# Kernel optimization log

Hardware: AMD Instinct MI355X
Metric: run time of the kernel (lower is better)

The kernel has to match this reference:

```python
import jax, jax.numpy as jnp
import numpy as np

# Graph / model dims (see init_kwargs)
N = 50000          # nodes
E = 800000         # edges (before self loops)
IN, HID, OUT = 128, 64, 47
HEADS = (4, 4, 1)
SLOPE = 0.2        # PyG GATConv default negative_slope
# dropout p=0.6 in the torch module is a no-op in eval mode -> omitted


def _glorot(key, shape):
    fan_in = shape[0] if len(shape) == 2 else int(np.prod(shape))
    return jax.random.normal(key, shape, jnp.float32) / np.sqrt(fan_in)


def setup_inputs() -> dict:
    key = jax.random.key(0)
    ks = jax.random.split(key, 16)
    x = jax.random.normal(ks[0], (N, IN), jnp.float32)
    edge_index = jax.random.randint(ks[1], (2, E), 0, N)
    # layer dims: (in_dim, out_dim_per_head, heads)
    dims = [(IN, HID, HEADS[0]), (HID * HEADS[0], HID, HEADS[1]), (HID * HEADS[1], OUT, HEADS[2])]
    inp = {"x": x, "edge_index": edge_index}
    for i, (d_in, c, h) in enumerate(dims, start=1):
        inp[f"W{i}"] = _glorot(ks[3 * i], (d_in, h * c))
        inp[f"a{i}s"] = _glorot(ks[3 * i + 1], (h, c))
        inp[f"a{i}d"] = _glorot(ks[3 * i + 2], (h, c))
        inp[f"b{i}"] = jnp.zeros((h * c,), jnp.float32)
    return inp


def gat_layer(x, src, dst, W, a_s, a_d, b, h, c):
    # x: [N, d_in] -> per-head features [N, h, c]
    feat = (x @ W).reshape(N, h, c)
    # per-node attention logits [N, h]
    al_src = jnp.einsum('nhc,hc->nh', feat, a_s)
    al_dst = jnp.einsum('nhc,hc->nh', feat, a_d)
    # per-edge score, LeakyReLU (PyG: alpha = a_src[src] + a_dst[dst])
    e = jax.nn.leaky_relu(al_src[src] + al_dst[dst], SLOPE)  # [Etot, h]
    # segment softmax over incoming edges of each dst node
    emax = jax.ops.segment_max(e, dst, num_segments=N)       # [N, h]
    w = jnp.exp(e - emax[dst])
    denom = jax.ops.segment_sum(w, dst, num_segments=N)      # [N, h]
    alpha = w / denom[dst]                                   # [Etot, h]
    # weighted scatter-add aggregation
    out = jax.ops.segment_sum(alpha[:, :, None] * feat[src], dst, num_segments=N)
    return out.reshape(N, h * c) + b                         # concat heads + bias


def reference(x, edge_index, W1, a1s, a1d, b1, W2, a2s, a2d, b2, W3, a3s, a3d, b3):
    loop = jnp.arange(N, dtype=edge_index.dtype)
    src = jnp.concatenate([edge_index[0], loop])  # add_self_loops=True
    dst = jnp.concatenate([edge_index[1], loop])
    h = gat_layer(x, src, dst, W1, a1s, a1d, b1, HEADS[0], HID)
    h = jax.nn.elu(h)
    h = gat_layer(h, src, dst, W2, a2s, a2d, b2, HEADS[1], HID)
    h = jax.nn.elu(h)
    h = gat_layer(h, src, dst, W3, a3s, a3d, b3, HEADS[2], OUT)  # no elu on last layer
    return h
```

## Files before the change

kernel.cpp:

```cpp
#include <hip/hip_runtime.h>
#include <hip/hip_bf16.h>

#define NNODES 50000
#define NEDGES 800000
#define ETOT   (NNODES + NEDGES)
#define MTILES 3136
#define MPAD   (MTILES * 16)
#define NBLK   196

typedef __attribute__((ext_vector_type(8))) short short8;
typedef __attribute__((ext_vector_type(4))) float floatx4;
typedef __attribute__((ext_vector_type(2))) unsigned int uint2v;

__device__ __forceinline__ float bf2f(__hip_bfloat16 x) { return __bfloat162float(x); }
__device__ __forceinline__ __hip_bfloat16 f2bf(float f) { return __float2bfloat16(f); }
__device__ __forceinline__ float sane(float v, float c) {
  v = (v == v) ? v : 0.f;
  return fminf(fmaxf(v, -c), c);
}

__global__ void zero_int_kernel(int* __restrict__ p, int n) {
  int i = blockIdx.x * blockDim.x + threadIdx.x;
  if (i < n) p[i] = 0;
}
__global__ void fill_out_kernel(float* __restrict__ o, int n, float v) {
  int i = blockIdx.x * blockDim.x + threadIdx.x;
  if (i < n) o[i] = v;
}
__global__ void split_input_kernel(const float* __restrict__ in,
                                   __hip_bfloat16* __restrict__ hi,
                                   __hip_bfloat16* __restrict__ lo, int n) {
  int i = blockIdx.x * blockDim.x + threadIdx.x;
  if (i >= n) return;
  float v = sane(in[i], 1e4f);
  __hip_bfloat16 h = f2bf(v);
  hi[i] = h;
  lo[i] = f2bf(v - bf2f(h));
}
__global__ void zero_tail_kernel(__hip_bfloat16* __restrict__ hi,
                                 __hip_bfloat16* __restrict__ lo) {
  const int base = NNODES * 128;
  const int cnt = MPAD * 256 - base;
  int i = blockIdx.x * blockDim.x + threadIdx.x;
  if (i >= cnt) return;
  hi[base + i] = f2bf(0.f);
  lo[base + i] = f2bf(0.f);
}
__global__ void pad47_kernel(const float* __restrict__ a, const float* __restrict__ b,
                             float* __restrict__ ap, float* __restrict__ bp) {
  int i = threadIdx.x;
  ap[i] = (i < 47) ? sane(a[i], 1e4f) : 0.f;
  bp[i] = (i < 47) ? sane(b[i], 1e4f) : 0.f;
}

__global__ void degree_kernel(const int* __restrict__ ei, int* __restrict__ deg) {
  int p = blockIdx.x * blockDim.x + threadIdx.x;
  if (p >= ETOT) return;
  int dst = (p < NEDGES) ? ei[NEDGES + p] : (p - NEDGES);
  dst = min(max(dst, 0), NNODES - 1);
  atomicAdd(&deg[dst], 1);
}

__global__ __launch_bounds__(256) void block_sum_kernel(const int* __restrict__ deg,
                                                        int* __restrict__ bsum) {
  __shared__ int sh[256];
  int b = blockIdx.x, t = threadIdx.x;
  int i = b * 256 + t;
  sh[t] = (i < NNODES) ? deg[i] : 0;
  __syncthreads();
  for (int off = 128; off > 0; off >>= 1) {
    if (t < off) sh[t] += sh[t + off];
    __syncthreads();
  }
  if (t == 0) bsum[b] = sh[0];
}

__global__ __launch_bounds__(256) void scan_bsum_kernel(const int* __restrict__ bsum,
                                                        int* __restrict__ boff,
                                                        int* __restrict__ row_ptr) {
  __shared__ int sh[256];
  int t = threadIdx.x;
  int v = (t < NBLK) ? bsum[t] : 0;
  sh[t] = v;
  __syncthreads();
  for (int off = 1; off < 256; off <<= 1) {
    int u = (t >= off) ? sh[t - off] : 0;
    __syncthreads();
    sh[t] += u;
    __syncthreads();
  }
  if (t < NBLK) boff[t] = sh[t] - v;
  if (t == 255) row_ptr[NNODES] = sh[255];
}

__global__ __launch_bounds__(256) void emit_rowptr_kernel(const int* __restrict__ deg,
                                                          const int* __restrict__ boff,
                                                          int* __restrict__ row_ptr,
                                                          int* __restrict__ cursor) {
  __shared__ int sh[256];
  int b = blockIdx.x, t = threadIdx.x;
  int i = b * 256 + t;
  int d = (i < NNODES) ? deg[i] : 0;
  sh[t] = d;
  __syncthreads();
  for (int off = 1; off < 256; off <<= 1) {
    int u = (t >= off) ? sh[t - off] : 0;
    __syncthreads();
    sh[t] += u;
    __syncthreads();
  }
  if (i < NNODES) {
    int v = boff[b] + sh[t] - d;
    row_ptr[i] = v;
    cursor[i] = v;
  }
}

__global__ void scatter_kernel(const int* __restrict__ ei, int* __restrict__ cursor,
                               int* __restrict__ csr_src) {
  int p = blockIdx.x * blockDim.x + threadIdx.x;
  if (p >= ETOT) return;
  int src, dst;
  if (p < NEDGES) { src = ei[p]; dst = ei[NEDGES + p]; }
  else            { src = p - NEDGES; dst = src; }
  src = min(max(src, 0), NNODES - 1);
  dst = min(max(dst, 0), NNODES - 1);
  int pos = atomicAdd(&cursor[dst], 1);
  pos = min(max(pos, 0), ETOT - 1);
  csr_src[pos] = src;
}

__global__ void pack_w_kernel(const float* __restrict__ W,
                              __hip_bfloat16* __restrict__ Bh,
                              __hip_bfloat16* __restrict__ Bl,
                              int K, int Nreal, int Npad) {
  int idx = blockIdx.x * blockDim.x + threadIdx.x;
  if (idx >= Npad * K) return;
  int e = idx;
  int j = e & 7;    e >>= 3;
  int m = e & 15;   e >>= 4;
  int quad = e & 3; e >>= 2;
  int kch = K >> 5;
  int kk32 = e % kch;
  int nt = e / kch;
  int n = nt * 16 + m;
  int k = kk32 * 32 + quad * 8 + j;
  float v = (n < Nreal) ? sane(W[k * Nreal + n], 1e4f) : 0.f;
  __hip_bfloat16 h = f2bf(v);
  Bh[idx] = h;
  Bl[idx] = f2bf(v - bf2f(h));
}

template<int KDIM, int NOUT, int HEADS, int WAVES_N>
__global__ __launch_bounds__(256) void gemm_attn_kernel(
    const __hip_bfloat16* __restrict__ Ah, const __hip_bfloat16* __restrict__ Al,
    const __hip_bfloat16* __restrict__ Bh, const __hip_bfloat16* __restrict__ Bl,
    const float* __restrict__ asv, const float* __restrict__ adv,
    __hip_bfloat16* __restrict__ Ch, float* __restrict__ als, float* __restrict__ ald) {
  constexpr int KCH = KDIM / 32;
  constexpr int CT = (NOUT / 16) / WAVES_N;
  constexpr int RT = 4;
  constexpr int RGROUPS = 4 / WAVES_N;
  __shared__ __hip_bfloat16 sAh[64 * 32];
  __shared__ __hip_bfloat16 sAl[64 * 32];
  int wave = threadIdx.x >> 6, lane = threadIdx.x & 63;
  int wrow = wave / WAVES_N, wcol = wave % WAVES_N;
  int rt0 = (blockIdx.x * RGROUPS + wrow) * RT;
  int ct0 = wcol * CT;
  int m = lane & 15, quad = lane >> 4;

  const short8* Bph = reinterpret_cast<const short8*>(Bh);
  const short8* Bpl = reinterpret_cast<const short8*>(Bl);

  floatx4 acc[RT][CT];
#pragma unroll
  for (int rt = 0; rt < RT; ++rt)
#pragma unroll
    for (int ct = 0; ct < CT; ++ct) acc[rt][ct] = (floatx4){0.f, 0.f, 0.f, 0.f};

  int tid = threadIdx.x;
  size_t gstage = (size_t)(rt0 * 16 + (tid >> 2)) * KDIM + (tid & 3) * 8;

#pragma unroll 2
  for (int kk = 0; kk < KCH; ++kk) {
    short8 a_h[RT], a_l[RT];
    if constexpr (WAVES_N == 4) {
      short8 vh = *reinterpret_cast<const short8*>(Ah + gstage + kk * 32);
      short8 vl = *reinterpret_cast<const short8*>(Al + gstage + kk * 32);
      __syncthreads();
      *reinterpret_cast<short8*>(&sAh[tid * 8]) = vh;
      *reinterpret_cast<short8*>(&sAl[tid * 8]) = vl;
      __syncthreads();
#pragma unroll
      for (int rt = 0; rt < RT; ++rt) {
        int so = (rt * 16 + m) * 32 + quad * 8;
        a_h[rt] = *reinterpret_cast<const short8*>(&sAh[so]);
        a_l[rt] = *reinterpret_cast<const short8*>(&sAl[so]);
      }
    } else {
#pragma unroll
      for (int rt = 0; rt < RT; ++rt) {
        size_t aoff = (size_t)((rt0 + rt) * 16 + m) * KDIM + kk * 32 + quad * 8;
        a_h[rt] = *reinterpret_cast<const short8*>(Ah + aoff);
        a_l[rt] = *reinterpret_cast<const short8*>(Al + aoff);
      }
    }
#pragma unroll
    for (int ct = 0; ct < CT; ++ct) {
      size_t o = ((size_t)(ct0 + ct) * KCH + kk) * 64 + lane;
      short8 b_h = Bph[o];
      short8 b_l = Bpl[o];
#pragma unroll
      for (int rt = 0; rt < RT; ++rt) {
        acc[rt][ct] = __builtin_amdgcn_mfma_f32_16x16x32_bf16(a_h[rt], b_h, acc[rt][ct], 0, 0, 0);
        acc[rt][ct] = __builtin_amdgcn_mfma_f32_16x16x32_bf16(a_h[rt], b_l, acc[rt][ct], 0, 0, 0);
        acc[rt][ct] = __builtin_amdgcn_mfma_f32_16x16x32_bf16(a_l[rt], b_h, acc[rt][ct], 0, 0, 0);
      }
    }
  }

  constexpr int CPH = NOUT / HEADS;
  int head = (ct0 * 16) / CPH;
  float asl[CT], adl[CT];
#pragma unroll
  for (int ct = 0; ct < CT; ++ct) {
    asl[ct] = asv[(ct0 + ct) * 16 + m];
    adl[ct] = adv[(ct0 + ct) * 16 + m];
  }
  float ps[RT * 4], pd[RT * 4];
#pragma unroll
  for (int i = 0; i < RT * 4; ++i) { ps[i] = 0.f; pd[i] = 0.f; }
#pragma unroll
  for (int rt = 0; rt < RT; ++rt)
#pragma unroll
    for (int ct = 0; ct < CT; ++ct)
#pragma unroll
      for (int r = 0; r < 4; ++r) {
        ps[rt * 4 + r] += acc[rt][ct][r] * asl[ct];
        pd[rt * 4 + r] += acc[rt][ct][r] * adl[ct];
      }
#pragma unroll
  for (int off = 1; off < 16; off <<= 1) {
#pragma unroll
    for (int i = 0; i < RT * 4; ++i) {
      ps[i] += __shfl_xor(ps[i], off);
      pd[i] += __shfl_xor(pd[i], off);
    }
  }
  if (m == 0) {
#pragma unroll
    for (int rt = 0; rt < RT; ++rt)
#pragma unroll
      for (int r = 0; r < 4; ++r) {
        int row = (rt0 + rt) * 16 + quad * 4 + r;
        if (row < NNODES) {
          als[(size_t)row * HEADS + head] = sane(ps[rt * 4 + r], 80.f);
          ald[(size_t)row * HEADS + head] = sane(pd[rt * 4 + r], 80.f);
        }
      }
  }

#pragma unroll
  for (int rt = 0; rt < RT; ++rt)
#pragma unroll
    for (int ct = 0; ct < CT; ++ct)
#pragma unroll
      for (int r = 0; r < 4; ++r) {
        int row = (rt0 + rt) * 16 + quad * 4 + r;
        if (row < NNODES) {
          float v = sane(acc[rt][ct][r], 3e4f);
          Ch[(size_t)row * NOUT + (ct0 + ct) * 16 + m] = f2bf(v);
        }
      }
}

template<int H>
__global__ __launch_bounds__(256) void alpha_kernel(const int* __restrict__ row_ptr,
                                                    const int* __restrict__ csr_src,
                                                    const float* __restrict__ als,
                                                    const float* __restrict__ ald,
                                                    float* __restrict__ alpha) {
  int wid = threadIdx.x >> 6, lane = threadIdx.x & 63;
  int dst = blockIdx.x * 4 + wid;
  if (dst >= NNODES) return;
  int start = row_ptr[dst], end = row_ptr[dst + 1];
  int cnt = end - start;
  if (cnt <= 0) return;
  float adv[H];
#pragma unroll
  for (int h = 0; h < H; ++h) adv[h] = ald[(size_t)dst * H + h];

  if (cnt <= 64) {
    int i = start + lane;
    bool valid = lane < cnt;
    int s = valid ? min(max(csr_src[i], 0), NNODES - 1) : 0;
    float w[H];
#pragma unroll
    for (int h = 0; h < H; ++h) {
      float e = als[(size_t)s * H + h] + adv[h];
      e = e > 0.f ? e : 0.2f * e;
      e = fminf(fmaxf(e, -80.f), 80.f);
      w[h] = valid ? __expf(e) : 0.f;
    }
#pragma unroll
    for (int h = 0; h < H; ++h) {
      float v = w[h];
#pragma unroll
      for (int off = 1; off < 64; off <<= 1) v += __shfl_xor(v, off);
      float inv = 1.f / fmaxf(v, 1e-30f);
      if (valid) alpha[(size_t)i * H + h] = w[h] * inv;
    }
  } else {
    float dl[H];
#pragma unroll
    for (int h = 0; h < H; ++h) dl[h] = 0.f;
    for (int base = start; base < end; base += 64) {
      int i = base + lane;
      bool valid = i < end;
      int s = valid ? min(max(csr_src[i], 0), NNODES - 1) : 0;
#pragma unroll
      for (int h = 0; h < H; ++h) {
        float e = als[(size_t)s * H + h] + adv[h];
        e = e > 0.f ? e : 0.2f * e;
        e = fminf(fmaxf(e, -80.f), 80.f);
        float w = valid ? __expf(e) : 0.f;
        dl[h] += w;
        if (valid) alpha[(size_t)i * H + h] = w;
      }
    }
    float inv[H];
#pragma unroll
    for (int h = 0; h < H; ++h) {
      float v = dl[h];
#pragma unroll
      for (int off = 1; off < 64; off <<= 1) v += __shfl_xor(v, off);
      inv[h] = 1.f / fmaxf(v, 1e-30f);
    }
    for (int base = start; base < end; base += 64) {
      int i = base + lane;
      if (i < end)
#pragma unroll
        for (int h = 0; h < H; ++h) alpha[(size_t)i * H + h] *= inv[h];
    }
  }
}

__global__ __launch_bounds__(256) void agg_mid_kernel(const int* __restrict__ row_ptr,
                                                      const int* __restrict__ csr_src,
                                                      const __hip_bfloat16* __restrict__ Fh,
                                                      const float* __restrict__ alpha,
                                                      const float* __restrict__ bias,
                                                      __hip_bfloat16* __restrict__ Oh,
                                                      __hip_bfloat16* __restrict__ Ol) {
  __shared__ float part[4][256];
  int dst = blockIdx.x;
  int wid = threadIdx.x >> 6, lane = threadIdx.x & 63;
  int start = row_ptr[dst], end = row_ptr[dst + 1];
  int cnt = end - start;
  int head = lane >> 4;
  float a0 = 0.f, a1 = 0.f, a2 = 0.f, a3 = 0.f;
  int p = wid;
  for (; p + 4 < cnt; p += 8) {
    int e0 = start + p, e1 = start + p + 4;
    int s0 = csr_src[e0], s1 = csr_src[e1];
    float w0 = alpha[(size_t)e0 * 4 + head];
    float w1 = alpha[(size_t)e1 * 4 + head];
    uint2v f0 = *reinterpret_cast<const uint2v*>(Fh + (size_t)s0 * 256 + lane * 4);
    uint2v f1 = *reinterpret_cast<const uint2v*>(Fh + (size_t)s1 * 256 + lane * 4);
    a0 += w0 * __uint_as_float(f0.x << 16);
    a1 += w0 * __uint_as_float(f0.x & 0xffff0000u);
    a2 += w0 * __uint_as_float(f0.y << 16);
    a3 += w0 * __uint_as_float(f0.y & 0xffff0000u);
    a0 += w1 * __uint_as_float(f1.x << 16);
    a1 += w1 * __uint_as_float(f1.x & 0xffff0000u);
    a2 += w1 * __uint_as_float(f1.y << 16);
    a3 += w1 * __uint_as_float(f1.y & 0xffff0000u);
  }
  for (; p < cnt; p += 4) {
    int e0 = start + p;
    int s0 = csr_src[e0];
    float w0 = alpha[(size_t)e0 * 4 + head];
    uint2v f0 = *reinterpret_cast<const uint2v*>(Fh + (size_t)s0 * 256 + lane * 4);
    a0 += w0 * __uint_as_float(f0.x << 16);
    a1 += w0 * __uint_as_float(f0.x & 0xffff0000u);
    a2 += w0 * __uint_as_float(f0.y << 16);
    a3 += w0 * __uint_as_float(f0.y & 0xffff0000u);
  }
  *reinterpret_cast<floatx4*>(&part[wid][lane * 4]) = (floatx4){a0, a1, a2, a3};
  __syncthreads();
  int t = threadIdx.x;
  float o = part[0][t] + part[1][t] + part[2][t] + part[3][t] + bias[t];
  o = o > 0.f ? o : __expf(o) - 1.f;
  __hip_bfloat16 h = f2bf(o);
  Oh[(size_t)dst * 256 + t] = h;
  Ol[(size_t)dst * 256 + t] = f2bf(o - bf2f(h));
}

__global__ void agg_final_kernel(const int* __restrict__ row_ptr,
                                 const int* __restrict__ csr_src,
                                 const __hip_bfloat16* __restrict__ Fh,
                                 const float* __restrict__ alpha,
                                 const float* __restrict__ bias,
                                 float* __restrict__ out) {
  int wid = threadIdx.x >> 6, lane = threadIdx.x & 63;
  int dst = blockIdx.x * 4 + wid;
  if (dst >= NNODES) return;
  int start = row_ptr[dst], end = row_ptr[dst + 1];
  float acc = 0.f;
  int e = start;
  for (; e + 1 < end; e += 2) {
    int s0 = csr_src[e], s1 = csr_src[e + 1];
    float w0 = alpha[e], w1 = alpha[e + 1];
    float f0 = bf2f(Fh[(size_t)s0 * 64 + lane]);
    float f1 = bf2f(Fh[(size_t)s1 * 64 + lane]);
    acc += w0 * f0 + w1 * f1;
  }
  for (; e < end; ++e) {
    int s0 = csr_src[e];
    acc += alpha[e] * bf2f(Fh[(size_t)s0 * 64 + lane]);
  }
  if (lane < 47) out[(size_t)dst * 47 + lane] = acc + bias[lane];
}

extern "C" void kernel_launch(void* const* d_in, const int* in_sizes, int n_in,
                              void* d_out, int out_size, void* d_ws, size_t ws_size,
                              hipStream_t stream) {
  const float* x   = (const float*)d_in[0];
  const int* ei    = (const int*)d_in[1];
  const float* W1  = (const float*)d_in[2];
  const float* a1s = (const float*)d_in[3];
  const float* a1d = (const float*)d_in[4];
  const float* b1  = (const float*)d_in[5];
  const float* W2  = (const float*)d_in[6];
  const float* a2s = (const float*)d_in[7];
  const float* a2d = (const float*)d_in[8];
  const float* b2  = (const float*)d_in[9];
  const float* W3  = (const float*)d_in[10];
  const float* a3s = (const float*)d_in[11];
  const float* a3d = (const float*)d_in[12];
  const float* b3  = (const float*)d_in[13];
  float* out = (float*)d_out;
  (void)n_in; (void)in_sizes;

  char* base = (char*)d_ws;
  size_t off = 0;
  auto alloc = [&](size_t bytes) -> char* {
    off = (off + 255) & ~(size_t)255;
    char* p = base + off;
    off += bytes;
    return p;
  };
  int* deg     = (int*)alloc((size_t)NNODES * 4);
  int* cursor  = (int*)alloc((size_t)NNODES * 4);
  int* row_ptr = (int*)alloc((size_t)(NNODES + 1) * 4);
  int* csr_src = (int*)alloc((size_t)ETOT * 4);
  int* bsum    = (int*)alloc(256 * 4);
  int* boff    = (int*)alloc(256 * 4);
  float* als   = (float*)alloc((size_t)NNODES * 4 * 4);
  float* ald   = (float*)alloc((size_t)NNODES * 4 * 4);
  float* alpha = (float*)alloc((size_t)ETOT * 4 * 4);
  __hip_bfloat16* Ah = (__hip_bfloat16*)alloc((size_t)MPAD * 256 * 2);
  __hip_bfloat16* Al = (__hip_bfloat16*)alloc((size_t)MPAD * 256 * 2);
  __hip_bfloat16* Fh = (__hip_bfloat16*)alloc((size_t)NNODES * 256 * 2);
  __hip_bfloat16* wth = (__hip_bfloat16*)alloc((size_t)256 * 256 * 2);
  __hip_bfloat16* wtl = (__hip_bfloat16*)alloc((size_t)256 * 256 * 2);
  float* asv3 = (float*)alloc(64 * 4);
  float* adv3 = (float*)alloc(64 * 4);

  if (ws_size < off) {
    fill_out_kernel<<<(out_size + 255) / 256, 256, 0, stream>>>(out, out_size, 12345.f);
    return;
  }

  zero_int_kernel<<<(NNODES + 255) / 256, 256, 0, stream>>>(deg, NNODES);
  degree_kernel<<<(ETOT + 255) / 256, 256, 0, stream>>>(ei, deg);
  block_sum_kernel<<<NBLK, 256, 0, stream>>>(deg, bsum);
  scan_bsum_kernel<<<1, 256, 0, stream>>>(bsum, boff, row_ptr);
  emit_rowptr_kernel<<<NBLK, 256, 0, stream>>>(deg, boff, row_ptr, cursor);
  scatter_kernel<<<(ETOT + 255) / 256, 256, 0, stream>>>(ei, cursor, csr_src);

  split_input_kernel<<<(NNODES * 128 + 255) / 256, 256, 0, stream>>>(x, Ah, Al, NNODES * 128);
  {
    const int tail = MPAD * 256 - NNODES * 128;
    zero_tail_kernel<<<(tail + 255) / 256, 256, 0, stream>>>(Ah, Al);
  }
  pad47_kernel<<<1, 64, 0, stream>>>(a3s, a3d, asv3, adv3);

  const int grid12 = (NNODES + 63) / 64;
  const int grid3 = (NNODES + 255) / 256;

  pack_w_kernel<<<(256 * 128 + 255) / 256, 256, 0, stream>>>(W1, wth, wtl, 128, 256, 256);
  gemm_attn_kernel<128, 256, 4, 4><<<grid12, 256, 0, stream>>>(Ah, Al, wth, wtl, a1s, a1d,
                                                               Fh, als, ald);
  alpha_kernel<4><<<(NNODES + 3) / 4, 256, 0, stream>>>(row_ptr, csr_src, als, ald, alpha);
  agg_mid_kernel<<<NNODES, 256, 0, stream>>>(row_ptr, csr_src, Fh, alpha, b1, Ah, Al);

  pack_w_kernel<<<(256 * 256 + 255) / 256, 256, 0, stream>>>(W2, wth, wtl, 256, 256, 256);
  gemm_attn_kernel<256, 256, 4, 4><<<grid12, 256, 0, stream>>>(Ah, Al, wth, wtl, a2s, a2d,
                                                               Fh, als, ald);
  alpha_kernel<4><<<(NNODES + 3) / 4, 256, 0, stream>>>(row_ptr, csr_src, als, ald, alpha);
  agg_mid_kernel<<<NNODES, 256, 0, stream>>>(row_ptr, csr_src, Fh, alpha, b2, Ah, Al);

  pack_w_kernel<<<(64 * 256 + 255) / 256, 256, 0, stream>>>(W3, wth, wtl, 256, 47, 64);
  gemm_attn_kernel<256, 64, 1, 1><<<grid3, 256, 0, stream>>>(Ah, Al, wth, wtl, asv3, adv3,
                                                             Fh, als, ald);
  alpha_kernel<1><<<(NNODES + 3) / 4, 256, 0, stream>>>(row_ptr, csr_src, als, ald, alpha);
  agg_final_kernel<<<(NNODES + 3) / 4, 256, 0, stream>>>(row_ptr, csr_src, Fh, alpha, b3, out);
}
```

Before: 574.8 us.

## Use one wave per node in aggregation, stage two K-chunks per sync, fuse tail zeroing

The mid-layer aggregation now gives each destination node one wave instead of a 256-thread block. This removes the shared-memory partial reduction and the block barrier, and the output is written as vectorized 4-element bf16 hi/lo stores. The GEMM stages two 32-wide K chunks per pair of barriers using a double-sized LDS buffer, which halves synchronization count. The edge loops are unrolled by 4 for more memory-level parallelism, and the tail-zero kernel is folded into the split-input kernel. The per-wave design trades intra-node parallelism for less sync overhead, and high-degree nodes now run serially in a single wave.

New measurement: 515.8 us. 10.3% less time.

```diff
diff --git a/kernel.cpp b/kernel.cpp
--- a/kernel.cpp
+++ b/kernel.cpp
@@ -11,6 +11,7 @@
 typedef __attribute__((ext_vector_type(8))) short short8;
 typedef __attribute__((ext_vector_type(4))) float floatx4;
 typedef __attribute__((ext_vector_type(2))) unsigned int uint2v;
+typedef __attribute__((ext_vector_type(4))) short short4v;
 
 __device__ __forceinline__ float bf2f(__hip_bfloat16 x) { return __bfloat162float(x); }
 __device__ __forceinline__ __hip_bfloat16 f2bf(float f) { return __float2bfloat16(f); }
@@ -18,6 +19,11 @@
   v = (v == v) ? v : 0.f;
   return fminf(fmaxf(v, -c), c);
 }
+__device__ __forceinline__ unsigned short bfbits(float f) {
+  union { __hip_bfloat16 b; unsigned short u; } cv;
+  cv.b = f2bf(f);
+  return cv.u;
+}
 
 __global__ void zero_int_kernel(int* __restrict__ p, int n) {
   int i = blockIdx.x * blockDim.x + threadIdx.x;
@@ -29,22 +35,13 @@
 }
 __global__ void split_input_kernel(const float* __restrict__ in,
                                    __hip_bfloat16* __restrict__ hi,
-                                   __hip_bfloat16* __restrict__ lo, int n) {
+                                   __hip_bfloat16* __restrict__ lo) {
   int i = blockIdx.x * blockDim.x + threadIdx.x;
-  if (i >= n) return;
-  float v = sane(in[i], 1e4f);
+  if (i >= MPAD * 256) return;
+  float v = (i < NNODES * 128) ? sane(in[i], 1e4f) : 0.f;
   __hip_bfloat16 h = f2bf(v);
   hi[i] = h;
   lo[i] = f2bf(v - bf2f(h));
-}
-__global__ void zero_tail_kernel(__hip_bfloat16* __restrict__ hi,
-                                 __hip_bfloat16* __restrict__ lo) {
-  const int base = NNODES * 128;
-  const int cnt = MPAD * 256 - base;
-  int i = blockIdx.x * blockDim.x + threadIdx.x;
-  if (i >= cnt) return;
-  hi[base + i] = f2bf(0.f);
-  lo[base + i] = f2bf(0.f);
 }
 __global__ void pad47_kernel(const float* __restrict__ a, const float* __restrict__ b,
                              float* __restrict__ ap, float* __restrict__ bp) {
@@ -161,8 +158,8 @@
   constexpr int CT = (NOUT / 16) / WAVES_N;
   constexpr int RT = 4;
   constexpr int RGROUPS = 4 / WAVES_N;
-  __shared__ __hip_bfloat16 sAh[64 * 32];
-  __shared__ __hip_bfloat16 sAl[64 * 32];
+  __shared__ __hip_bfloat16 sAh[2 * 64 * 32];
+  __shared__ __hip_bfloat16 sAl[2 * 64 * 32];
   int wave = threadIdx.x >> 6, lane = threadIdx.x & 63;
   int wrow = wave / WAVES_N, wcol = wave % WAVES_N;
   int rt0 = (blockIdx.x * RGROUPS + wrow) * RT;
@@ -182,39 +179,63 @@
   size_t gstage = (size_t)(rt0 * 16 + (tid >> 2)) * KDIM + (tid & 3) * 8;
 
 #pragma unroll 2
-  for (int kk = 0; kk < KCH; ++kk) {
+  for (int ks = 0; ks < KCH / 2; ++ks) {
     short8 a_h[RT], a_l[RT];
     if constexpr (WAVES_N == 4) {
-      short8 vh = *reinterpret_cast<const short8*>(Ah + gstage + kk * 32);
-      short8 vl = *reinterpret_cast<const short8*>(Al + gstage + kk * 32);
+      short8 vh0 = *reinterpret_cast<const short8*>(Ah + gstage + ks * 64);
+      short8 vh1 = *reinterpret_cast<const short8*>(Ah + gstage + ks * 64 + 32);
+      short8 vl0 = *reinterpret_cast<const short8*>(Al + gstage + ks * 64);
+      short8 vl1 = *reinterpret_cast<const short8*>(Al + gstage + ks * 64 + 32);
       __syncthreads();
-      *reinterpret_cast<short8*>(&sAh[tid * 8]) = vh;
-      *reinterpret_cast<short8*>(&sAl[tid * 8]) = vl;
+      *reinterpret_cast<short8*>(&sAh[tid * 8]) = vh0;
+      *reinterpret_cast<short8*>(&sAh[2048 + tid * 8]) = vh1;
+      *reinterpret_cast<short8*>(&sAl[tid * 8]) = vl0;
+      *reinterpret_cast<short8*>(&sAl[2048 + tid * 8]) = vl1;
       __syncthreads();
 #pragma unroll
-      for (int rt = 0; rt < RT; ++rt) {
-        int so = (rt * 16 + m) * 32 + quad * 8;
-        a_h[rt] = *reinterpret_cast<const short8*>(&sAh[so]);
-        a_l[rt] = *reinterpret_cast<const short8*>(&sAl[so]);
+      for (int kk0 = 0; kk0 < 2; ++kk0) {
+#pragma unroll
+        for (int rt = 0; rt < RT; ++rt) {
+          int so = kk0 * 2048 + (rt * 16 + m) * 32 + quad * 8;
+          a_h[rt] = *reinterpret_cast<const short8*>(&sAh[so]);
+          a_l[rt] = *reinterpret_cast<const short8*>(&sAl[so]);
+        }
+        int kk = ks * 2 + kk0;
+#pragma unroll
+        for (int ct = 0; ct < CT; ++ct) {
+          size_t o = ((size_t)(ct0 + ct) * KCH + kk) * 64 + lane;
+          short8 b_h = Bph[o];
+          short8 b_l = Bpl[o];
+#pragma unroll
+          for (int rt = 0; rt < RT; ++rt) {
+            acc[rt][ct] = __builtin_amdgcn_mfma_f32_16x16x32_bf16(a_h[rt], b_h, acc[rt][ct], 0, 0, 0);
+            acc[rt][ct] = __builtin_amdgcn_mfma_f32_16x16x32_bf16(a_h[rt], b_l, acc[rt][ct], 0, 0, 0);
+            acc[rt][ct] = __builtin_amdgcn_mfma_f32_16x16x32_bf16(a_l[rt], b_h, acc[rt][ct], 0, 0, 0);
+          }
+        }
       }
     } else {
 #pragma unroll
-      for (int rt = 0; rt < RT; ++rt) {
-        size_t aoff = (size_t)((rt0 + rt) * 16 + m) * KDIM + kk * 32 + quad * 8;
-        a_h[rt] = *reinterpret_cast<const short8*>(Ah + aoff);
-        a_l[rt] = *reinterpret_cast<const short8*>(Al + aoff);
-      }
-    }
-#pragma unroll
-    for (int ct = 0; ct < CT; ++ct) {
-      size_t o = ((size_t)(ct0 + ct) * KCH + kk) * 64 + lane;
-      short8 b_h = Bph[o];
-      short8 b_l = Bpl[o];
-#pragma unroll
-      for (int rt = 0; rt < RT; ++rt) {
-        acc[rt][ct] = __builtin_amdgcn_mfma_f32_16x16x32_bf16(a_h[rt], b_h, acc[rt][ct], 0, 0, 0);
-        acc[rt][ct] = __builtin_amdgcn_mfma_f32_16x16x32_bf16(a_h[rt], b_l, acc[rt][ct], 0, 0, 0);
-        acc[rt][ct] = __builtin_amdgcn_mfma_f32_16x16x32_bf16(a_l[rt], b_h, acc[rt][ct], 0, 0, 0);
+      for (int kk0 = 0; kk0 < 2; ++kk0) {
+        int kk = ks * 2 + kk0;
+#pragma unroll
+        for (int rt = 0; rt < RT; ++rt) {
+          size_t aoff = (size_t)((rt0 + rt) * 16 + m) * KDIM + kk * 32 + quad * 8;
+          a_h[rt] = *reinterpret_cast<const short8*>(Ah + aoff);
+          a_l[rt] = *reinterpret_cast<const short8*>(Al + aoff);
+        }
+#pragma unroll
+        for (int ct = 0; ct < CT; ++ct) {
+          size_t o = ((size_t)(ct0 + ct) * KCH + kk) * 64 + lane;
+          short8 b_h = Bph[o];
+          short8 b_l = Bpl[o];
+#pragma unroll
+          for (int rt = 0; rt < RT; ++rt) {
+            acc[rt][ct] = __builtin_amdgcn_mfma_f32_16x16x32_bf16(a_h[rt], b_h, acc[rt][ct], 0, 0, 0);
+            acc[rt][ct] = __builtin_amdgcn_mfma_f32_16x16x32_bf16(a_h[rt], b_l, acc[rt][ct], 0, 0, 0);
+            acc[rt][ct] = __builtin_amdgcn_mfma_f32_16x16x32_bf16(a_l[rt], b_h, acc[rt][ct], 0, 0, 0);
+          }
+        }
       }
     }
   }
@@ -352,21 +373,25 @@
                                                       const float* __restrict__ bias,
                                                       __hip_bfloat16* __restrict__ Oh,
                                                       __hip_bfloat16* __restrict__ Ol) {
-  __shared__ float part[4][256];
-  int dst = blockIdx.x;
   int wid = threadIdx.x >> 6, lane = threadIdx.x & 63;
+  int dst = blockIdx.x * 4 + wid;
+  if (dst >= NNODES) return;
   int start = row_ptr[dst], end = row_ptr[dst + 1];
   int cnt = end - start;
   int head = lane >> 4;
   float a0 = 0.f, a1 = 0.f, a2 = 0.f, a3 = 0.f;
-  int p = wid;
-  for (; p + 4 < cnt; p += 8) {
-    int e0 = start + p, e1 = start + p + 4;
-    int s0 = csr_src[e0], s1 = csr_src[e1];
+  int p = 0;
+  for (; p + 3 < cnt; p += 4) {
+    int e0 = start + p, e1 = e0 + 1, e2 = e0 + 2, e3 = e0 + 3;
+    int s0 = csr_src[e0], s1 = csr_src[e1], s2 = csr_src[e2], s3 = csr_src[e3];
     float w0 = alpha[(size_t)e0 * 4 + head];
     float w1 = alpha[(size_t)e1 * 4 + head];
+    float w2 = alpha[(size_t)e2 * 4 + head];
+    float w3 = alpha[(size_t)e3 * 4 + head];
     uint2v f0 = *reinterpret_cast<const uint2v*>(Fh + (size_t)s0 * 256 + lane * 4);
     uint2v f1 = *reinterpret_cast<const uint2v*>(Fh + (size_t)s1 * 256 + lane * 4);
+    uint2v f2 = *reinterpret_cast<const uint2v*>(Fh + (size_t)s2 * 256 + lane * 4);
+    uint2v f3 = *reinterpret_cast<const uint2v*>(Fh + (size_t)s3 * 256 + lane * 4);
     a0 += w0 * __uint_as_float(f0.x << 16);
     a1 += w0 * __uint_as_float(f0.x & 0xffff0000u);
     a2 += w0 * __uint_as_float(f0.y << 16);
@@ -375,8 +400,16 @@
     a1 += w1 * __uint_as_float(f1.x & 0xffff0000u);
     a2 += w1 * __uint_as_float(f1.y << 16);
     a3 += w1 * __uint_as_float(f1.y & 0xffff0000u);
-  }
-  for (; p < cnt; p += 4) {
+    a0 += w2 * __uint_as_float(f2.x << 16);
+    a1 += w2 * __uint_as_float(f2.x & 0xffff0000u);
+    a2 += w2 * __uint_as_float(f2.y << 16);
+    a3 += w2 * __uint_as_float(f2.y & 0xffff0000u);
+    a0 += w3 * __uint_as_float(f3.x << 16);
+    a1 += w3 * __uint_as_float(f3.x & 0xffff0000u);
+    a2 += w3 * __uint_as_float(f3.y << 16);
+    a3 += w3 * __uint_as_float(f3.y & 0xffff0000u);
+  }
+  for (; p < cnt; ++p) {
     int e0 = start + p;
     int s0 = csr_src[e0];
     float w0 = alpha[(size_t)e0 * 4 + head];
@@ -386,14 +419,18 @@
     a2 += w0 * __uint_as_float(f0.y << 16);
     a3 += w0 * __uint_as_float(f0.y & 0xffff0000u);
   }
-  *reinterpret_cast<floatx4*>(&part[wid][lane * 4]) = (floatx4){a0, a1, a2, a3};
-  __syncthreads();
-  int t = threadIdx.x;
-  float o = part[0][t] + part[1][t] + part[2][t] + part[3][t] + bias[t];
-  o = o > 0.f ? o : __expf(o) - 1.f;
-  __hip_bfloat16 h = f2bf(o);
-  Oh[(size_t)dst * 256 + t] = h;
-  Ol[(size_t)dst * 256 + t] = f2bf(o - bf2f(h));
+  floatx4 bv = *reinterpret_cast<const floatx4*>(bias + lane * 4);
+  float o0 = a0 + bv.x, o1 = a1 + bv.y, o2 = a2 + bv.z, o3 = a3 + bv.w;
+  o0 = o0 > 0.f ? o0 : __expf(o0) - 1.f;
+  o1 = o1 > 0.f ? o1 : __expf(o1) - 1.f;
+  o2 = o2 > 0.f ? o2 : __expf(o2) - 1.f;
+  o3 = o3 > 0.f ? o3 : __expf(o3) - 1.f;
+  float h0 = bf2f(f2bf(o0)), h1 = bf2f(f2bf(o1)), h2 = bf2f(f2bf(o2)), h3 = bf2f(f2bf(o3));
+  short4v hv = (short4v){(short)bfbits(o0), (short)bfbits(o1), (short)bfbits(o2), (short)bfbits(o3)};
+  short4v lv = (short4v){(short)bfbits(o0 - h0), (short)bfbits(o1 - h1),
+                         (short)bfbits(o2 - h2), (short)bfbits(o3 - h3)};
+  *reinterpret_cast<short4v*>(Oh + (size_t)dst * 256 + lane * 4) = hv;
+  *reinterpret_cast<short4v*>(Ol + (size_t)dst * 256 + lane * 4) = lv;
 }
 
 __global__ void agg_final_kernel(const int* __restrict__ row_ptr,
@@ -406,18 +443,22 @@
   int dst = blockIdx.x * 4 + wid;
   if (dst >= NNODES) return;
   int start = row_ptr[dst], end = row_ptr[dst + 1];
+  int cnt = end - start;
   float acc = 0.f;
-  int e = start;
-  for (; e + 1 < end; e += 2) {
-    int s0 = csr_src[e], s1 = csr_src[e + 1];
-    float w0 = alpha[e], w1 = alpha[e + 1];
+  int p = 0;
+  for (; p + 3 < cnt; p += 4) {
+    int e0 = start + p;
+    int s0 = csr_src[e0], s1 = csr_src[e0 + 1], s2 = csr_src[e0 + 2], s3 = csr_src[e0 + 3];
+    float w0 = alpha[e0], w1 = alpha[e0 + 1], w2 = alpha[e0 + 2], w3 = alpha[e0 + 3];
     float f0 = bf2f(Fh[(size_t)s0 * 64 + lane]);
     float f1 = bf2f(Fh[(size_t)s1 * 64 + lane]);
-    acc += w0 * f0 + w1 * f1;
-  }
-  for (; e < end; ++e) {
-    int s0 = csr_src[e];
-    acc += alpha[e] * bf2f(Fh[(size_t)s0 * 64 + lane]);
+    float f2 = bf2f(Fh[(size_t)s2 * 64 + lane]);
+    float f3 = bf2f(Fh[(size_t)s3 * 64 + lane]);
+    acc += w0 * f0 + w1 * f1 + w2 * f2 + w3 * f3;
+  }
+  for (; p < cnt; ++p) {
+    int e0 = start + p;
+    acc += alpha[e0] * bf2f(Fh[(size_t)csr_src[e0] * 64 + lane]);
   }
   if (lane < 47) out[(size_t)dst * 47 + lane] = acc + bias[lane];
 }
@@ -479,31 +520,28 @@
   emit_rowptr_kernel<<<NBLK, 256, 0, stream>>>(deg, boff, row_ptr, cursor);
   scatter_kernel<<<(ETOT + 255) / 256, 256, 0, stream>>>(ei, cursor, csr_src);
 
-  split_input_kernel<<<(NNODES * 128 + 255) / 256, 256, 0, stream>>>(x, Ah, Al, NNODES * 128);
-  {
-    const int tail = MPAD * 256 - NNODES * 128;
-    zero_tail_kernel<<<(tail + 255) / 256, 256, 0, stream>>>(Ah, Al);
-  }
+  split_input_kernel<<<(MPAD * 256 + 255) / 256, 256, 0, stream>>>(x, Ah, Al);
   pad47_kernel<<<1, 64, 0, stream>>>(a3s, a3d, asv3, adv3);
 
   const int grid12 = (NNODES + 63) / 64;
   const int grid3 = (NNODES + 255) / 256;
+  const int gridN4 = (NNODES + 3) / 4;
 
   pack_w_kernel<<<(256 * 128 + 255) / 256, 256, 0, stream>>>(W1, wth, wtl, 128, 256, 256);
   gemm_attn_kernel<128, 256, 4, 4><<<grid12, 256, 0, stream>>>(Ah, Al, wth, wtl, a1s, a1d,
                                                                Fh, als, ald);
-  alpha_kernel<4><<<(NNODES + 3) / 4, 256, 0, stream>>>(row_ptr, csr_src, als, ald, alpha);
-  agg_mid_kernel<<<NNODES, 256, 0, stream>>>(row_ptr, csr_src, Fh, alpha, b1, Ah, Al);
+  alpha_kernel<4><<<gridN4, 256, 0, stream>>>(row_ptr, csr_src, als, ald, alpha);
+  agg_mid_kernel<<<gridN4, 256, 0, stream>>>(row_ptr, csr_src, Fh, alpha, b1, Ah, Al);
 
   pack_w_kernel<<<(256 * 256 + 255) / 256, 256, 0, stream>>>(W2, wth, wtl, 256, 256, 256);
   gemm_attn_kernel<256, 256, 4, 4><<<grid12, 256, 0, stream>>>(Ah, Al, wth, wtl, a2s, a2d,
                                                                Fh, als, ald);
-  alpha_kernel<4><<<(NNODES + 3) / 4, 256, 0, stream>>>(row_ptr, csr_src, als, ald, alpha);
-  agg_mid_kernel<<<NNODES, 256, 0, stream>>>(row_ptr, csr_src, Fh, alpha, b2, Ah, Al);
+  alpha_kernel<4><<<gridN4, 256, 0, stream>>>(row_ptr, csr_src, als, ald, alpha);
+  agg_mid_kernel<<<gridN4, 256, 0, stream>>>(row_ptr, csr_src, Fh, alpha, b2, Ah, Al);
 
   pack_w_kernel<<<(64 * 256 + 255) / 256, 256, 0, stream>>>(W3, wth, wtl, 256, 47, 64);
   gemm_attn_kernel<256, 64, 1, 1><<<grid3, 256, 0, stream>>>(Ah, Al, wth, wtl, asv3, adv3,
                                                              Fh, als, ald);
-  alpha_kernel<1><<<(NNODES + 3) / 4, 256, 0, stream>>>(row_ptr, csr_src, als, ald, alpha);
-  agg_final_kernel<<<(NNODES + 3) / 4, 256, 0, stream>>>(row_ptr, csr_src, Fh, alpha, b3, out);
-}
+  alpha_kernel<1><<<gridN4, 256, 0, stream>>>(row_ptr, csr_src, als, ald, alpha);
+  agg_final_kernel<<<gridN4, 256, 0, stream>>>(row_ptr, csr_src, Fh, alpha, b3, out);
+}
```
